# Kernel tuning notes

Hardware: AMD Instinct MI355X
Metric: run time of the kernel (lower is better)

The kernel has to match this reference:

```python
import jax, jax.numpy as jnp
import numpy as np
import math

D = 1024      # model dim
H = 16        # heads
DK = D // H   # 64
FF = 4096     # ff_dim
B, T = 2, 2048


def _norm(x, alpha, bias, eps=1e-6):
    # torch: (x - mean) / (x.std(unbiased) + eps) * alpha + bias
    mu = jnp.mean(x, axis=-1, keepdims=True)
    sd = jnp.std(x, axis=-1, keepdims=True, ddof=1)  # unbiased, like torch
    return alpha * ((x - mu) / (sd + eps)) + bias


def setup_inputs() -> dict:
    key = jax.random.key(0)
    ks = jax.random.split(key, 20)
    w = lambda k, shp: (jax.random.normal(k, shp, jnp.float32) * 0.02)
    inp = {
        "x": jax.random.normal(ks[0], (B, T, D), jnp.float32),
        "x_mask": jnp.ones((B, T), jnp.int32),  # unused by the module's forward
        "Wq": w(ks[1], (D, D)), "bq": jnp.zeros((D,), jnp.float32),
        "Wk": w(ks[2], (D, D)), "bk": jnp.zeros((D,), jnp.float32),
        "Wv": w(ks[3], (D, D)), "bv": jnp.zeros((D,), jnp.float32),
        "Wo": w(ks[4], (D, D)), "bo": jnp.zeros((D,), jnp.float32),
        "W1": w(ks[5], (D, FF)), "b1": jnp.zeros((FF,), jnp.float32),
        "W2": w(ks[6], (FF, D)), "b2": jnp.zeros((D,), jnp.float32),
        "alpha1": jnp.ones((D,), jnp.float32), "beta1": jnp.zeros((D,), jnp.float32),
        "alpha2": jnp.ones((D,), jnp.float32), "beta2": jnp.zeros((D,), jnp.float32),
    }
    return inp


def reference(x, x_mask, Wq, bq, Wk, bk, Wv, bv, Wo, bo,
              W1, b1, W2, b2, alpha1, beta1, alpha2, beta2):
    b, t, d = x.shape
    # projections -> [B, H, T, DK]
    q = (x @ Wq + bq).reshape(b, t, H, DK).swapaxes(1, 2)
    k = (x @ Wk + bk).reshape(b, t, H, DK).swapaxes(1, 2)
    v = (x @ Wv + bv).reshape(b, t, H, DK).swapaxes(1, 2)
    # eager attention: QK^T / sqrt(dk), clamp_min(-6000), softmax (no mask used)
    score = jnp.einsum('bhqd,bhkd->bhqk', q, k) / math.sqrt(DK)
    score = jnp.maximum(score, -6000.0)
    score = jax.nn.softmax(score, axis=-1)  # dropout=identity at inference
    val = jnp.einsum('bhqk,bhkd->bhqd', score, v)
    val = val.swapaxes(1, 2).reshape(b, t, d)
    attn_out = val @ Wo + bo
    # residual + norm1 (dropout identity)
    xn = _norm(x + attn_out, alpha1, beta1)
    # FFN: relu(linear1) -> linear2
    ff = jnp.maximum(xn @ W1 + b1, 0.0) @ W2 + b2
    out = _norm(xn + ff, alpha2, beta2)
    return out, score
```

## Files before the change

### kernel.cpp

```cpp
#include <hip/hip_runtime.h>
#include <stdint.h>

#define T_SEQ   2048
#define D_MODEL 1024
#define N_HEADS 16
#define D_HEAD  64
#define FF_DIM  4096
#define BATCH   2
#define BT      (BATCH * T_SEQ)

typedef unsigned short u16;
typedef __attribute__((ext_vector_type(8))) short bf16x8;
typedef __attribute__((ext_vector_type(4))) float f32x4;
typedef __attribute__((ext_vector_type(16))) float f32x16;

__device__ __forceinline__ u16 f2bf(float f) {
  union { float f; unsigned u; } x; x.f = f;
  unsigned r = x.u + 0x7fffu + ((x.u >> 16) & 1u);
  return (u16)(r >> 16);
}

__device__ __forceinline__ void gload16(const void* g, void* l) {
  __builtin_amdgcn_global_load_lds(
      (const __attribute__((address_space(1))) void*)g,
      (__attribute__((address_space(3))) void*)l, 16, 0, 0);
}

struct PrepArgs {
  const float* x; u16* xb;
  const float *Wq, *Wk, *Wv, *Wo, *W1, *W2;
  u16 *WqT, *WkT, *WvT, *WoT, *W1T, *W2T;
};

__global__ __launch_bounds__(256)
void prep_kernel(PrepArgs pa) {
  const int bid = blockIdx.x;
  const int tid = threadIdx.x;
  if (bid < 4096) {
    int i = (bid * 256 + tid) * 4;
    float4 v = *(const float4*)(pa.x + i);
    ushort4 o; o.x = f2bf(v.x); o.y = f2bf(v.y); o.z = f2bf(v.z); o.w = f2bf(v.w);
    *(ushort4*)(pa.xb + i) = o;
    return;
  }
  int t = bid - 4096;
  const float* W; u16* Wt; int K, N, rel;
  if (t < 1024)      { W = pa.Wq; Wt = pa.WqT; K = 1024; N = 1024; rel = t; }
  else if (t < 2048) { W = pa.Wk; Wt = pa.WkT; K = 1024; N = 1024; rel = t - 1024; }
  else if (t < 3072) { W = pa.Wv; Wt = pa.WvT; K = 1024; N = 1024; rel = t - 2048; }
  else if (t < 4096) { W = pa.Wo; Wt = pa.WoT; K = 1024; N = 1024; rel = t - 3072; }
  else if (t < 8192) { W = pa.W1; Wt = pa.W1T; K = 1024; N = 4096; rel = t - 4096; }
  else               { W = pa.W2; Wt = pa.W2T; K = 4096; N = 1024; rel = t - 8192; }
  const int ntn = N >> 5;
  const int n0 = (rel % ntn) * 32, k0 = (rel / ntn) * 32;
  const int tx = tid & 31, ty = tid >> 5;
  __shared__ float tile[32][33];
#pragma unroll
  for (int r = 0; r < 4; ++r)
    tile[ty + r * 8][tx] = W[(size_t)(k0 + ty + r * 8) * N + n0 + tx];
  __syncthreads();
#pragma unroll
  for (int r = 0; r < 4; ++r)
    Wt[(size_t)(n0 + ty + r * 8) * K + k0 + tx] = f2bf(tile[tx][ty + r * 8]);
}

struct GemmArgs {
  const u16* A;
  const u16* B0; const u16* B1; const u16* B2;
  const float* bias0; const float* bias1; const float* bias2;
  void* out0; void* out1; void* out2;
  int M, N, K;
};

template <int EPI>
__global__ __launch_bounds__(256, 3)
void gemm_bt(GemmArgs ga) {
  const int tid = threadIdx.x;
  const int gx = gridDim.x, gy = gridDim.y;
  const int nwg = gx * gy * gridDim.z;
  const int orig = blockIdx.x + gx * (blockIdx.y + gy * blockIdx.z);
  const int swz = (orig & 7) * (nwg >> 3) + (orig >> 3);
  const int bx = swz % gx, by = (swz / gx) % gy, bz = swz / (gx * gy);
  const int m0 = by * 128;
  const int n0 = bx * 128;
  const int lane = tid & 63, w = tid >> 6;
  const int wr = w >> 1, wc = w & 1;
  const int l15 = lane & 15, g = lane >> 4;

  const u16* Bt; const float* bias; void* outp;
  int z = 0;
  if (EPI == 0) {
    z = bz;
    Bt   = (z == 0) ? ga.B0   : (z == 1) ? ga.B1   : ga.B2;
    bias = (z == 0) ? ga.bias0 : (z == 1) ? ga.bias1 : ga.bias2;
    outp = (z == 0) ? ga.out0 : (z == 1) ? ga.out1 : ga.out2;
  } else if (EPI == 3) {
    z = bz; Bt = ga.B0; bias = nullptr; outp = ga.out0;
  } else { Bt = ga.B0; bias = ga.bias0; outp = ga.out0; }

  __shared__ char lsA[128 * 128];
  __shared__ char lsB[128 * 128];

  f32x4 acc[4][4] = {};
  const int K = ga.K;
  const int kbase = (EPI == 3) ? z * (K >> 1) : 0;
  const int nk = (EPI == 3) ? (K >> 7) : (K >> 6);

  auto stage = [&](int kt) {
    const int k0 = kbase + kt * 64;
#pragma unroll
    for (int i = 0; i < 4; ++i) {
      int o = i * 4096 + tid * 16;
      int row = o >> 7, cb = o & 127;
      int lcb = cb ^ ((row & 7) << 4);
      gload16((const char*)ga.A + ((size_t)(m0 + row) * K + k0) * 2 + lcb, lsA + o);
    }
#pragma unroll
    for (int i = 0; i < 4; ++i) {
      int o = i * 4096 + tid * 16;
      int row = o >> 7, cb = o & 127;
      int lcb = cb ^ ((row & 7) << 4);
      gload16((const char*)Bt + ((size_t)(n0 + row) * K + k0) * 2 + lcb, lsB + o);
    }
  };

  stage(0);
  for (int kt = 0; kt < nk; ++kt) {
    __syncthreads();
#pragma unroll
    for (int kk = 0; kk < 2; ++kk) {
      bf16x8 a[4], b[4];
#pragma unroll
      for (int mi = 0; mi < 4; ++mi) {
        int row = wr * 64 + mi * 16 + l15;
        a[mi] = *(const bf16x8*)(lsA + row * 128 + ((kk * 64 + g * 16) ^ ((row & 7) << 4)));
      }
#pragma unroll
      for (int ni = 0; ni < 4; ++ni) {
        int row = wc * 64 + ni * 16 + l15;
        b[ni] = *(const bf16x8*)(lsB + row * 128 + ((kk * 64 + g * 16) ^ ((row & 7) << 4)));
      }
#pragma unroll
      for (int mi = 0; mi < 4; ++mi)
#pragma unroll
        for (int ni = 0; ni < 4; ++ni)
          acc[mi][ni] = __builtin_amdgcn_mfma_f32_16x16x32_bf16(a[mi], b[ni], acc[mi][ni], 0, 0, 0);
    }
    __syncthreads();
    if (kt + 1 < nk) stage(kt + 1);
  }

  const int N = ga.N;
#pragma unroll
  for (int mi = 0; mi < 4; ++mi) {
#pragma unroll
    for (int ni = 0; ni < 4; ++ni) {
      const int c = n0 + wc * 64 + ni * 16 + l15;
      const float bv = (EPI == 3) ? 0.0f : bias[c];
#pragma unroll
      for (int j = 0; j < 4; ++j) {
        const int r = m0 + wr * 64 + mi * 16 + g * 4 + j;
        float v = acc[mi][ni][j] + bv;
        if constexpr (EPI == 0) {
          const int bb = r >> 11, t = r & 2047, hh = c >> 6, dk = c & 63;
          u16* o = (u16*)outp;
          size_t idx = (z < 2)
              ? ((size_t)((bb * N_HEADS + hh) * T_SEQ + t)) * D_HEAD + dk
              : ((size_t)((bb * N_HEADS + hh) * D_HEAD + dk)) * T_SEQ + t;
          o[idx] = f2bf(v);
        } else if constexpr (EPI == 3) {
          ((float*)outp)[(size_t)z * ga.M * N + (size_t)r * N + c] = v;
        } else {
          ((u16*)outp)[(size_t)r * N + c] = f2bf(fmaxf(v, 0.0f));
        }
      }
    }
  }
}

__global__ __launch_bounds__(128, 2)
void attn_kernel(const u16* __restrict__ q, const u16* __restrict__ k,
                 const u16* __restrict__ vT, float* __restrict__ score,
                 u16* __restrict__ val) {
  const int tid = threadIdx.x;
  const int lane = tid & 63, w = tid >> 6;
  const int l31 = lane & 31, hi = lane >> 5;
  const int nwg = gridDim.x;
  const int orig = blockIdx.x;
  const int swz = (orig & 7) * (nwg >> 3) + (orig >> 3);
  const int bh = swz >> 5;
  const int Q0 = (swz & 31) * 64;
  const size_t hoff = (size_t)bh * T_SEQ * D_HEAD;
  const u16* qb = q + hoff;
  const u16* kb = k + hoff;
  const u16* vb = vT + hoff;
  float* sb = score + ((size_t)bh * T_SEQ + Q0) * T_SEQ;

  __shared__ char lsK[128 * 128];
  __shared__ char lsV[64 * 256];
  __shared__ char lsP[2][32 * 128];

  auto stageK = [&](int jt) {
    const int J0 = jt * 128;
#pragma unroll
    for (int i = 0; i < 8; ++i) {
      int o = i * 2048 + tid * 16;
      int row = o >> 7, cb = o & 127;
      int lcb = cb ^ ((row & 7) << 4);
      gload16((const char*)kb + ((size_t)(J0 + row) * D_HEAD) * 2 + lcb, lsK + o);
    }
  };
  auto stageV = [&](int jt) {
    const int J0 = jt * 128;
#pragma unroll
    for (int i = 0; i < 8; ++i) {
      int o = i * 2048 + tid * 16;
      int row = o >> 8, cb = o & 255;
      int lcb = cb ^ ((row & 15) << 4);
      gload16((const char*)vb + ((size_t)row * T_SEQ + J0) * 2 + lcb, lsV + o);
    }
  };

  bf16x8 qf[4];
  {
    int row = Q0 + w * 32 + l31;
#pragma unroll
    for (int ks = 0; ks < 4; ++ks)
      qf[ks] = *(const bf16x8*)(qb + (size_t)row * D_HEAD + ks * 16 + hi * 8);
  }

  float lsum[16];
#pragma unroll
  for (int r = 0; r < 16; ++r) lsum[r] = 0.f;

  for (int jt = 0; jt < 16; ++jt) {
    __syncthreads();
    stageK(jt);
    __syncthreads();
#pragma unroll
    for (int st = 0; st < 4; ++st) {
      f32x16 c = {};
      __builtin_amdgcn_s_setprio(1);
#pragma unroll
      for (int ks = 0; ks < 4; ++ks) {
        int row = st * 32 + l31;
        bf16x8 b = *(const bf16x8*)(lsK + row * 128 + ((ks * 32 + hi * 16) ^ ((row & 7) << 4)));
        c = __builtin_amdgcn_mfma_f32_32x32x16_bf16(qf[ks], b, c, 0, 0, 0);
      }
      __builtin_amdgcn_s_setprio(0);
#pragma unroll
      for (int r = 0; r < 16; ++r)
        lsum[r] += __expf(fmaxf(c[r] * 0.125f, -6000.0f));
    }
  }
  float inv[16];
#pragma unroll
  for (int r = 0; r < 16; ++r) {
    float v = lsum[r];
    v += __shfl_xor(v, 1);
    v += __shfl_xor(v, 2);
    v += __shfl_xor(v, 4);
    v += __shfl_xor(v, 8);
    v += __shfl_xor(v, 16);
    inv[r] = 1.0f / v;
  }

  f32x16 vacc[2] = {};
  char* myP = lsP[w];

  for (int jt = 0; jt < 16; ++jt) {
    const int J0 = jt * 128;
    __syncthreads();
    stageK(jt);
    stageV(jt);
    __syncthreads();
#pragma unroll
    for (int h = 0; h < 2; ++h) {
#pragma unroll
      for (int st = 0; st < 2; ++st) {
        f32x16 c = {};
        __builtin_amdgcn_s_setprio(1);
#pragma unroll
        for (int ks = 0; ks < 4; ++ks) {
          int row = h * 64 + st * 32 + l31;
          bf16x8 b = *(const bf16x8*)(lsK + row * 128 + ((ks * 32 + hi * 16) ^ ((row & 7) << 4)));
          c = __builtin_amdgcn_mfma_f32_32x32x16_bf16(qf[ks], b, c, 0, 0, 0);
        }
        __builtin_amdgcn_s_setprio(0);
#pragma unroll
        for (int r = 0; r < 16; ++r) {
          int rr = (r & 3) + 8 * (r >> 2) + 4 * hi;
          float p = __expf(fmaxf(c[r] * 0.125f, -6000.0f)) * inv[r];
          __builtin_nontemporal_store(
              p, &sb[(size_t)(w * 32 + rr) * T_SEQ + J0 + h * 64 + st * 32 + l31]);
          *(u16*)(myP + rr * 128 + (((st * 32 + l31) * 2) ^ ((rr & 7) << 4))) = f2bf(p);
        }
      }
#pragma unroll
      for (int ks = 0; ks < 4; ++ks) {
        bf16x8 pa = *(const bf16x8*)(myP + l31 * 128 + ((ks * 32 + hi * 16) ^ ((l31 & 7) << 4)));
        __builtin_amdgcn_s_setprio(1);
#pragma unroll
        for (int ct = 0; ct < 2; ++ct) {
          int vrow = ct * 32 + l31;
          bf16x8 vf = *(const bf16x8*)(lsV + vrow * 256 +
                                       ((h * 128 + ks * 32 + hi * 16) ^ ((vrow & 15) << 4)));
          vacc[ct] = __builtin_amdgcn_mfma_f32_32x32x16_bf16(pa, vf, vacc[ct], 0, 0, 0);
        }
        __builtin_amdgcn_s_setprio(0);
      }
    }
  }

  const int bb = bh >> 4, hh = bh & 15;
#pragma unroll
  for (int ct = 0; ct < 2; ++ct)
#pragma unroll
    for (int r = 0; r < 16; ++r) {
      int rr = (r & 3) + 8 * (r >> 2) + 4 * hi;
      int qrow = Q0 + w * 32 + rr;
      val[((size_t)(bb * T_SEQ + qrow)) * D_MODEL + hh * D_HEAD + ct * 32 + l31] =
          f2bf(vacc[ct][r]);
    }
}

template <bool WRITE_BF16>
__global__ __launch_bounds__(256)
void norm_kernel(const float* __restrict__ p0, const float* __restrict__ p1,
                 const float* __restrict__ bias, const float* __restrict__ resid,
                 const float* __restrict__ alpha, const float* __restrict__ beta,
                 float* __restrict__ outf, u16* __restrict__ outb) {
  const int row = blockIdx.x;
  const int tid = threadIdx.x;
  const size_t base = (size_t)row * D_MODEL + tid * 4;
  float4 v0 = *(const float4*)(p0 + base);
  float4 v1 = *(const float4*)(p1 + base);
  float4 bi = *(const float4*)(bias + tid * 4);
  float4 rs = *(const float4*)(resid + base);
  float4 v;
  v.x = v0.x + v1.x + bi.x + rs.x;
  v.y = v0.y + v1.y + bi.y + rs.y;
  v.z = v0.z + v1.z + bi.z + rs.z;
  v.w = v0.w + v1.w + bi.w + rs.w;
  float s = v.x + v.y + v.z + v.w;
  float ss = v.x * v.x + v.y * v.y + v.z * v.z + v.w * v.w;
#pragma unroll
  for (int m = 1; m < 64; m <<= 1) {
    s += __shfl_xor(s, m);
    ss += __shfl_xor(ss, m);
  }
  __shared__ float red[8];
  int w = tid >> 6, lane = tid & 63;
  if (lane == 0) { red[w] = s; red[4 + w] = ss; }
  __syncthreads();
  s = red[0] + red[1] + red[2] + red[3];
  ss = red[4] + red[5] + red[6] + red[7];
  float mu = s * (1.0f / 1024.0f);
  float var = fmaxf(ss - s * mu, 0.0f) * (1.0f / 1023.0f);
  float inv = 1.0f / (sqrtf(var) + 1e-6f);
  float4 a = *(const float4*)(alpha + tid * 4);
  float4 be = *(const float4*)(beta + tid * 4);
  float4 o;
  o.x = (v.x - mu) * inv * a.x + be.x;
  o.y = (v.y - mu) * inv * a.y + be.y;
  o.z = (v.z - mu) * inv * a.z + be.z;
  o.w = (v.w - mu) * inv * a.w + be.w;
  *(float4*)(outf + base) = o;
  if (WRITE_BF16) {
    ushort4 ob; ob.x = f2bf(o.x); ob.y = f2bf(o.y); ob.z = f2bf(o.z); ob.w = f2bf(o.w);
    *(ushort4*)(outb + base) = ob;
  }
}

extern "C" void kernel_launch(void* const* d_in, const int* in_sizes, int n_in,
                              void* d_out, int out_size, void* d_ws, size_t ws_size,
                              hipStream_t stream) {
  const float* x   = (const float*)d_in[0];
  const float* Wq  = (const float*)d_in[2];
  const float* bq  = (const float*)d_in[3];
  const float* Wk  = (const float*)d_in[4];
  const float* bk  = (const float*)d_in[5];
  const float* Wv  = (const float*)d_in[6];
  const float* bv  = (const float*)d_in[7];
  const float* Wo  = (const float*)d_in[8];
  const float* bo  = (const float*)d_in[9];
  const float* W1  = (const float*)d_in[10];
  const float* b1  = (const float*)d_in[11];
  const float* W2  = (const float*)d_in[12];
  const float* b2  = (const float*)d_in[13];
  const float* a1  = (const float*)d_in[14];
  const float* be1 = (const float*)d_in[15];
  const float* a2  = (const float*)d_in[16];
  const float* be2 = (const float*)d_in[17];

  float* out   = (float*)d_out;
  float* score = out + (size_t)BT * D_MODEL;

  char* ws = (char*)d_ws;
  const size_t MB = (size_t)1 << 20;
  u16*   xb   = (u16*)(ws + 0 * MB);
  u16*   WqT  = (u16*)(ws + 8 * MB);
  u16*   WkT  = (u16*)(ws + 10 * MB);
  u16*   WvT  = (u16*)(ws + 12 * MB);
  u16*   WoT  = (u16*)(ws + 14 * MB);
  u16*   W1T  = (u16*)(ws + 16 * MB);
  u16*   W2T  = (u16*)(ws + 24 * MB);
  u16*   qw   = (u16*)(ws + 32 * MB);
  u16*   kw   = (u16*)(ws + 40 * MB);
  u16*   vTw  = (u16*)(ws + 48 * MB);
  u16*   valw = (u16*)(ws + 56 * MB);
  float* p0   = (float*)(ws + 64 * MB);
  float* p1   = (float*)(ws + 80 * MB);
  float* xn   = (float*)(ws + 0 * MB);
  u16*   xnb  = (u16*)(ws + 96 * MB);
  u16*   hw   = (u16*)(ws + 32 * MB);

  {
    PrepArgs pa{ x, xb, Wq, Wk, Wv, Wo, W1, W2, WqT, WkT, WvT, WoT, W1T, W2T };
    prep_kernel<<<16384, 256, 0, stream>>>(pa);
  }

  {
    GemmArgs ga{};
    ga.A = xb;
    ga.B0 = WqT; ga.B1 = WkT; ga.B2 = WvT;
    ga.bias0 = bq; ga.bias1 = bk; ga.bias2 = bv;
    ga.out0 = qw; ga.out1 = kw; ga.out2 = vTw;
    ga.M = BT; ga.N = D_MODEL; ga.K = D_MODEL;
    gemm_bt<0><<<dim3(8, 32, 3), 256, 0, stream>>>(ga);
  }

  attn_kernel<<<1024, 128, 0, stream>>>(qw, kw, vTw, score, valw);

  {
    GemmArgs ga{};
    ga.A = valw; ga.B0 = WoT; ga.out0 = p0;
    ga.M = BT; ga.N = D_MODEL; ga.K = D_MODEL;
    gemm_bt<3><<<dim3(8, 32, 2), 256, 0, stream>>>(ga);
  }

  norm_kernel<true><<<BT, 256, 0, stream>>>(p0, p0 + (size_t)BT * D_MODEL, bo, x,
                                            a1, be1, xn, xnb);

  {
    GemmArgs ga{};
    ga.A = xnb; ga.B0 = W1T; ga.bias0 = b1; ga.out0 = hw;
    ga.M = BT; ga.N = FF_DIM; ga.K = D_MODEL;
    gemm_bt<2><<<dim3(32, 32, 1), 256, 0, stream>>>(ga);
  }

  {
    GemmArgs ga{};
    ga.A = hw; ga.B0 = W2T; ga.out0 = p0;
    ga.M = BT; ga.N = D_MODEL; ga.K = FF_DIM;
    gemm_bt<3><<<dim3(8, 32, 2), 256, 0, stream>>>(ga);
  }

  norm_kernel<false><<<BT, 256, 0, stream>>>(p0, p0 + (size_t)BT * D_MODEL, b2, xn,
                                             a2, be2, out, nullptr);
}
```

Before: 342.2 us.

## Split attention over key halves into separate denominator and PV kernels

The single attention kernel is replaced by two kernels. The first computes the partial softmax denominators for each half of the keys. The second recomputes the scores, normalizes them with the summed denominators, writes the score matrix and produces a partial PV result per key half. Together they double the number of workgroups and shrink LDS per block so occupancy can rise. The Wo projection now consumes the two partial value tensors as its split inputs, each over the full K, and the norm kernel adds them. The cost is extra workspace traffic for the partial values and a larger Wo GEMM.

```diff
diff --git a/kernel.cpp b/kernel.cpp
--- a/kernel.cpp
+++ b/kernel.cpp
@@ -87,6 +87,7 @@
   const int wr = w >> 1, wc = w & 1;
   const int l15 = lane & 15, g = lane >> 4;
 
+  const u16* Ap = ga.A;
   const u16* Bt; const float* bias; void* outp;
   int z = 0;
   if (EPI == 0) {
@@ -96,6 +97,9 @@
     outp = (z == 0) ? ga.out0 : (z == 1) ? ga.out1 : ga.out2;
   } else if (EPI == 3) {
     z = bz; Bt = ga.B0; bias = nullptr; outp = ga.out0;
+  } else if (EPI == 4) {
+    z = bz; Bt = ga.B0; bias = nullptr; outp = ga.out0;
+    if (z == 1) Ap = ga.B1;
   } else { Bt = ga.B0; bias = ga.bias0; outp = ga.out0; }
 
   __shared__ char lsA[128 * 128];
@@ -113,7 +117,7 @@
       int o = i * 4096 + tid * 16;
       int row = o >> 7, cb = o & 127;
       int lcb = cb ^ ((row & 7) << 4);
-      gload16((const char*)ga.A + ((size_t)(m0 + row) * K + k0) * 2 + lcb, lsA + o);
+      gload16((const char*)Ap + ((size_t)(m0 + row) * K + k0) * 2 + lcb, lsA + o);
     }
 #pragma unroll
     for (int i = 0; i < 4; ++i) {
@@ -156,7 +160,7 @@
 #pragma unroll
     for (int ni = 0; ni < 4; ++ni) {
       const int c = n0 + wc * 64 + ni * 16 + l15;
-      const float bv = (EPI == 3) ? 0.0f : bias[c];
+      const float bv = (EPI == 3 || EPI == 4) ? 0.0f : bias[c];
 #pragma unroll
       for (int j = 0; j < 4; ++j) {
         const int r = m0 + wr * 64 + mi * 16 + g * 4 + j;
@@ -168,7 +172,7 @@
               ? ((size_t)((bb * N_HEADS + hh) * T_SEQ + t)) * D_HEAD + dk
               : ((size_t)((bb * N_HEADS + hh) * D_HEAD + dk)) * T_SEQ + t;
           o[idx] = f2bf(v);
-        } else if constexpr (EPI == 3) {
+        } else if constexpr (EPI == 3 || EPI == 4) {
           ((float*)outp)[(size_t)z * ga.M * N + (size_t)r * N + c] = v;
         } else {
           ((u16*)outp)[(size_t)r * N + c] = f2bf(fmaxf(v, 0.0f));
@@ -178,67 +182,50 @@
   }
 }
 
-__global__ __launch_bounds__(128, 2)
-void attn_kernel(const u16* __restrict__ q, const u16* __restrict__ k,
-                 const u16* __restrict__ vT, float* __restrict__ score,
-                 u16* __restrict__ val) {
+
+__global__ __launch_bounds__(128, 4)
+void attn_den(const u16* __restrict__ q, const u16* __restrict__ k,
+              float* __restrict__ den) {
   const int tid = threadIdx.x;
   const int lane = tid & 63, w = tid >> 6;
   const int l31 = lane & 31, hi = lane >> 5;
   const int nwg = gridDim.x;
   const int orig = blockIdx.x;
   const int swz = (orig & 7) * (nwg >> 3) + (orig >> 3);
-  const int bh = swz >> 5;
-  const int Q0 = (swz & 31) * 64;
+  const int bh = swz >> 6;
+  const int Q0 = ((swz >> 1) & 31) * 64;
+  const int jh = swz & 1;
   const size_t hoff = (size_t)bh * T_SEQ * D_HEAD;
   const u16* qb = q + hoff;
   const u16* kb = k + hoff;
-  const u16* vb = vT + hoff;
-  float* sb = score + ((size_t)bh * T_SEQ + Q0) * T_SEQ;
-
-  __shared__ char lsK[128 * 128];
-  __shared__ char lsV[64 * 256];
-  __shared__ char lsP[2][32 * 128];
-
-  auto stageK = [&](int jt) {
-    const int J0 = jt * 128;
-#pragma unroll
-    for (int i = 0; i < 8; ++i) {
+
+  __shared__ char lsK[64 * 128];
+
+  bf16x8 qf[4];
+  {
+    int row = Q0 + w * 32 + l31;
+#pragma unroll
+    for (int ks = 0; ks < 4; ++ks)
+      qf[ks] = *(const bf16x8*)(qb + (size_t)row * D_HEAD + ks * 16 + hi * 8);
+  }
+
+  float lsum[16];
+#pragma unroll
+  for (int r = 0; r < 16; ++r) lsum[r] = 0.f;
+
+  for (int jt = 0; jt < 16; ++jt) {
+    const int J0 = jh * 1024 + jt * 64;
+    __syncthreads();
+#pragma unroll
+    for (int i = 0; i < 4; ++i) {
       int o = i * 2048 + tid * 16;
       int row = o >> 7, cb = o & 127;
       int lcb = cb ^ ((row & 7) << 4);
       gload16((const char*)kb + ((size_t)(J0 + row) * D_HEAD) * 2 + lcb, lsK + o);
     }
-  };
-  auto stageV = [&](int jt) {
-    const int J0 = jt * 128;
-#pragma unroll
-    for (int i = 0; i < 8; ++i) {
-      int o = i * 2048 + tid * 16;
-      int row = o >> 8, cb = o & 255;
-      int lcb = cb ^ ((row & 15) << 4);
-      gload16((const char*)vb + ((size_t)row * T_SEQ + J0) * 2 + lcb, lsV + o);
-    }
-  };
-
-  bf16x8 qf[4];
-  {
-    int row = Q0 + w * 32 + l31;
-#pragma unroll
-    for (int ks = 0; ks < 4; ++ks)
-      qf[ks] = *(const bf16x8*)(qb + (size_t)row * D_HEAD + ks * 16 + hi * 8);
-  }
-
-  float lsum[16];
-#pragma unroll
-  for (int r = 0; r < 16; ++r) lsum[r] = 0.f;
-
-  for (int jt = 0; jt < 16; ++jt) {
     __syncthreads();
-    stageK(jt);
-    __syncthreads();
-#pragma unroll
-    for (int st = 0; st < 4; ++st) {
+#pragma unroll
+    for (int st = 0; st < 2; ++st) {
       f32x16 c = {};
       __builtin_amdgcn_s_setprio(1);
 #pragma unroll
@@ -253,7 +240,6 @@
         lsum[r] += __expf(fmaxf(c[r] * 0.125f, -6000.0f));
     }
   }
-  float inv[16];
 #pragma unroll
   for (int r = 0; r < 16; ++r) {
     float v = lsum[r];
@@ -262,64 +248,116 @@
     v += __shfl_xor(v, 4);
     v += __shfl_xor(v, 8);
     v += __shfl_xor(v, 16);
-    inv[r] = 1.0f / v;
+    if (l31 == 0) {
+      int rr = (r & 3) + 8 * (r >> 2) + 4 * hi;
+      den[((size_t)jh * 32 + bh) * T_SEQ + Q0 + w * 32 + rr] = v;
+    }
+  }
+}
+
+__global__ __launch_bounds__(128, 3)
+void attn_pv(const u16* __restrict__ q, const u16* __restrict__ k,
+             const u16* __restrict__ vT, const float* __restrict__ den,
+             float* __restrict__ score, u16* __restrict__ val) {
+  const int tid = threadIdx.x;
+  const int lane = tid & 63, w = tid >> 6;
+  const int l31 = lane & 31, hi = lane >> 5;
+  const int nwg = gridDim.x;
+  const int orig = blockIdx.x;
+  const int swz = (orig & 7) * (nwg >> 3) + (orig >> 3);
+  const int bh = swz >> 6;
+  const int Q0 = ((swz >> 1) & 31) * 64;
+  const int jh = swz & 1;
+  const size_t hoff = (size_t)bh * T_SEQ * D_HEAD;
+  const u16* qb = q + hoff;
+  const u16* kb = k + hoff;
+  const u16* vb = vT + hoff;
+  float* sb = score + ((size_t)bh * T_SEQ + Q0) * T_SEQ;
+
+  __shared__ char lsK[64 * 128];
+  __shared__ char lsV[64 * 128];
+  __shared__ char lsP[2][32 * 128];
+
+  bf16x8 qf[4];
+  {
+    int row = Q0 + w * 32 + l31;
+#pragma unroll
+    for (int ks = 0; ks < 4; ++ks)
+      qf[ks] = *(const bf16x8*)(qb + (size_t)row * D_HEAD + ks * 16 + hi * 8);
+  }
+
+  float inv[16];
+#pragma unroll
+  for (int r = 0; r < 16; ++r) {
+    int rr = (r & 3) + 8 * (r >> 2) + 4 * hi;
+    size_t di = (size_t)bh * T_SEQ + Q0 + w * 32 + rr;
+    inv[r] = 1.0f / (den[di] + den[(size_t)32 * T_SEQ + di]);
   }
 
   f32x16 vacc[2] = {};
   char* myP = lsP[w];
 
   for (int jt = 0; jt < 16; ++jt) {
-    const int J0 = jt * 128;
+    const int J0 = jh * 1024 + jt * 64;
     __syncthreads();
-    stageK(jt);
-    stageV(jt);
+#pragma unroll
+    for (int i = 0; i < 4; ++i) {
+      int o = i * 2048 + tid * 16;
+      int row = o >> 7, cb = o & 127;
+      int lcb = cb ^ ((row & 7) << 4);
+      gload16((const char*)kb + ((size_t)(J0 + row) * D_HEAD) * 2 + lcb, lsK + o);
+    }
+#pragma unroll
+    for (int i = 0; i < 4; ++i) {
+      int o = i * 2048 + tid * 16;
+      int row = o >> 7, cb = o & 127;
+      int lcb = cb ^ ((row & 7) << 4);
+      gload16((const char*)vb + ((size_t)row * T_SEQ + J0) * 2 + lcb, lsV + o);
+    }
     __syncthreads();
 #pragma unroll
-    for (int h = 0; h < 2; ++h) {
-#pragma unroll
-      for (int st = 0; st < 2; ++st) {
-        f32x16 c = {};
-        __builtin_amdgcn_s_setprio(1);
-#pragma unroll
-        for (int ks = 0; ks < 4; ++ks) {
-          int row = h * 64 + st * 32 + l31;
-          bf16x8 b = *(const bf16x8*)(lsK + row * 128 + ((ks * 32 + hi * 16) ^ ((row & 7) << 4)));
-          c = __builtin_amdgcn_mfma_f32_32x32x16_bf16(qf[ks], b, c, 0, 0, 0);
-        }
-        __builtin_amdgcn_s_setprio(0);
-#pragma unroll
-        for (int r = 0; r < 16; ++r) {
-          int rr = (r & 3) + 8 * (r >> 2) + 4 * hi;
-          float p = __expf(fmaxf(c[r] * 0.125f, -6000.0f)) * inv[r];
-          __builtin_nontemporal_store(
-              p, &sb[(size_t)(w * 32 + rr) * T_SEQ + J0 + h * 64 + st * 32 + l31]);
-          *(u16*)(myP + rr * 128 + (((st * 32 + l31) * 2) ^ ((rr & 7) << 4))) = f2bf(p);
-        }
-      }
+    for (int st = 0; st < 2; ++st) {
+      f32x16 c = {};
+      __builtin_amdgcn_s_setprio(1);
 #pragma unroll
       for (int ks = 0; ks < 4; ++ks) {
-        bf16x8 pa = *(const bf16x8*)(myP + l31 * 128 + ((ks * 32 + hi * 16) ^ ((l31 & 7) << 4)));
-        __builtin_amdgcn_s_setprio(1);
-#pragma unroll
-        for (int ct = 0; ct < 2; ++ct) {
-          int vrow = ct * 32 + l31;
-          bf16x8 vf = *(const bf16x8*)(lsV + vrow * 256 +
-                                       ((h * 128 + ks * 32 + hi * 16) ^ ((vrow & 15) << 4)));
-          vacc[ct] = __builtin_amdgcn_mfma_f32_32x32x16_bf16(pa, vf, vacc[ct], 0, 0, 0);
-        }
-        __builtin_amdgcn_s_setprio(0);
-      }
+        int row = st * 32 + l31;
+        bf16x8 b = *(const bf16x8*)(lsK + row * 128 + ((ks * 32 + hi * 16) ^ ((row & 7) << 4)));
+        c = __builtin_amdgcn_mfma_f32_32x32x16_bf16(qf[ks], b, c, 0, 0, 0);
+      }
+      __builtin_amdgcn_s_setprio(0);
+#pragma unroll
+      for (int r = 0; r < 16; ++r) {
+        int rr = (r & 3) + 8 * (r >> 2) + 4 * hi;
+        float p = __expf(fmaxf(c[r] * 0.125f, -6000.0f)) * inv[r];
+        __builtin_nontemporal_store(
+            p, &sb[(size_t)(w * 32 + rr) * T_SEQ + J0 + st * 32 + l31]);
+        *(u16*)(myP + rr * 128 + (((st * 32 + l31) * 2) ^ ((rr & 7) << 4))) = f2bf(p);
+      }
+    }
+#pragma unroll
+    for (int ks = 0; ks < 4; ++ks) {
+      bf16x8 pa = *(const bf16x8*)(myP + l31 * 128 + ((ks * 32 + hi * 16) ^ ((l31 & 7) << 4)));
+      __builtin_amdgcn_s_setprio(1);
+#pragma unroll
+      for (int ct = 0; ct < 2; ++ct) {
+        int vrow = ct * 32 + l31;
+        bf16x8 vf = *(const bf16x8*)(lsV + vrow * 128 + ((ks * 32 + hi * 16) ^ ((vrow & 7) << 4)));
+        vacc[ct] = __builtin_amdgcn_mfma_f32_32x32x16_bf16(pa, vf, vacc[ct], 0, 0, 0);
+      }
+      __builtin_amdgcn_s_setprio(0);
     }
   }
 
   const int bb = bh >> 4, hh = bh & 15;
+  u16* vout = val + (size_t)jh * BT * D_MODEL;
 #pragma unroll
   for (int ct = 0; ct < 2; ++ct)
 #pragma unroll
     for (int r = 0; r < 16; ++r) {
       int rr = (r & 3) + 8 * (r >> 2) + 4 * hi;
       int qrow = Q0 + w * 32 + rr;
-      val[((size_t)(bb * T_SEQ + qrow)) * D_MODEL + hh * D_HEAD + ct * 32 + l31] =
+      vout[((size_t)(bb * T_SEQ + qrow)) * D_MODEL + hh * D_HEAD + ct * 32 + l31] =
           f2bf(vacc[ct][r]);
     }
 }
@@ -409,11 +447,12 @@
   u16*   kw   = (u16*)(ws + 40 * MB);
   u16*   vTw  = (u16*)(ws + 48 * MB);
   u16*   valw = (u16*)(ws + 56 * MB);
-  float* p0   = (float*)(ws + 64 * MB);
-  float* p1   = (float*)(ws + 80 * MB);
+  float* p0   = (float*)(ws + 72 * MB);
+  float* p1   = (float*)(ws + 88 * MB);
+  float* denw = (float*)(ws + 8 * MB);
   float* xn   = (float*)(ws + 0 * MB);
-  u16*   xnb  = (u16*)(ws + 96 * MB);
-  u16*   hw   = (u16*)(ws + 32 * MB);
+  u16*   xnb  = (u16*)(ws + 32 * MB);
+  u16*   hw   = (u16*)(ws + 40 * MB);
 
   {
     PrepArgs pa{ x, xb, Wq, Wk, Wv, Wo, W1, W2, WqT, WkT, WvT, WoT, W1T, W2T };
@@ -430,17 +469,21 @@
     gemm_bt<0><<<dim3(8, 32, 3), 256, 0, stream>>>(ga);
   }
 
-  attn_kernel<<<1024, 128, 0, stream>>>(qw, kw, vTw, score, valw);
+  attn_den<<<2048, 128, 0, stream>>>(qw, kw, denw);
+
+  attn_pv<<<2048, 128, 0, stream>>>(qw, kw, vTw, denw, score, valw);
 
   {
     GemmArgs ga{};
-    ga.A = valw; ga.B0 = WoT; ga.out0 = p0;
+    ga.A = valw;
+    ga.B0 = WoT;
+    ga.B1 = (const u16*)(valw + (size_t)BT * D_MODEL);
+    ga.out0 = p0;
     ga.M = BT; ga.N = D_MODEL; ga.K = D_MODEL;
-    gemm_bt<3><<<dim3(8, 32, 2), 256, 0, stream>>>(ga);
-  }
-
-  norm_kernel<true><<<BT, 256, 0, stream>>>(p0, p0 + (size_t)BT * D_MODEL, bo, x,
-                                            a1, be1, xn, xnb);
+    gemm_bt<4><<<dim3(8, 32, 2), 256, 0, stream>>>(ga);
+  }
+
+  norm_kernel<true><<<BT, 256, 0, stream>>>(p0, p1, bo, x, a1, be1, xn, xnb);
 
   {
     GemmArgs ga{};
@@ -456,6 +499,5 @@
     gemm_bt<3><<<dim3(8, 32, 2), 256, 0, stream>>>(ga);
   }
 
-  norm_kernel<false><<<BT, 256, 0, stream>>>(p0, p0 + (size_t)BT * D_MODEL, b2, xn,
-                                             a2, be2, out, nullptr);
-}
+  norm_kernel<false><<<BT, 256, 0, stream>>>(p0, p1, b2, xn, a2, be2, out, nullptr);
+}
```

After: 471.9 us. 37.9% more time.
